# Optimization experiments

Measured on AMD Instinct MI355X. Metric: run time of the kernel, lower is better.

The kernel has to match this reference:

```python
import jax, jax.numpy as jnp
import numpy as np
import math

HEADS = 8

def setup_inputs() -> dict:
    key = jax.random.key(0)
    k1, k2 = jax.random.split(key)
    B, C, H, W = 8, 512, 32, 32
    x = jax.random.normal(k1, (B, C, H, W), dtype=jnp.float32)
    # weight-norm 1x1 conv params: v ~ N(0, 0.05), g initialized to ||v|| (torch weight_norm default)
    proj_v = jax.random.normal(k2, (3 * C, C), dtype=jnp.float32) * 0.05
    proj_g = jnp.linalg.norm(proj_v, axis=1)
    proj_b = jnp.zeros((3 * C,), dtype=jnp.float32)
    return {"x": x, "proj_v": proj_v, "proj_g": proj_g, "proj_b": proj_b}

def reference(x, proj_v, proj_g, proj_b):
    B, C, H, W = x.shape
    heads = HEADS
    dim = C // heads
    N = H * W
    # weight-normalized 1x1 conv: w = g * v / ||v|| per output channel
    w = proj_g[:, None] * proj_v / jnp.linalg.norm(proj_v, axis=1, keepdims=True)
    c = jnp.einsum('oc,bchw->bohw', w, x) + proj_b[None, :, None, None]
    c = c.reshape(B, 3, heads, dim, N)
    q, k, v = c[:, 0], c[:, 1], c[:, 2]  # each (B, heads, dim, N)
    scale = 1.0 / math.sqrt(dim)
    attn = jnp.einsum('bhdq,bhdk->bhqk', q, k) * scale  # (B, heads, N, N)
    attn = jax.nn.softmax(attn, axis=-1)
    out = jnp.einsum('bhdk,bhqk->bhdq', v, attn)  # (B, heads, dim, N)
    return x + out.reshape(B, C, H, W)
```

## Files before the change

kernel.cpp:

```cpp
#include <hip/hip_runtime.h>

typedef _Float16 f16;
typedef _Float16 f16x2 __attribute__((ext_vector_type(2)));
typedef _Float16 f16x4 __attribute__((ext_vector_type(4)));
typedef _Float16 f16x8 __attribute__((ext_vector_type(8)));
typedef float f32x4 __attribute__((ext_vector_type(4)));
typedef unsigned int u32;

__device__ inline f32x4 mfma16(f16x8 a, f16x8 b, f32x4 c) {
    return __builtin_amdgcn_mfma_f32_16x16x32_f16(a, b, c, 0, 0, 0);
}

__device__ inline f16x2 pk2(float a, float b) {
    return __builtin_bit_cast(f16x2, __builtin_amdgcn_cvt_pkrtz(a, b));
}

__device__ inline void st8(f16* p, f16x8 v) {
    *(f16x4*)p = __builtin_shufflevector(v, v, 0, 1, 2, 3);
    *(f16x4*)(p + 4) = __builtin_shufflevector(v, v, 4, 5, 6, 7);
}
__device__ inline f16x8 ld8(const f16* p) {
    f16x4 lo = *(const f16x4*)p;
    f16x4 hi = *(const f16x4*)(p + 4);
    return __builtin_shufflevector(lo, hi, 0, 1, 2, 3, 4, 5, 6, 7);
}

__device__ inline void gl2lds16(const f16* g, f16* l) {
    __builtin_amdgcn_global_load_lds(
        (const __attribute__((address_space(1))) u32*)g,
        (__attribute__((address_space(3))) u32*)l, 16, 0, 0);
}

__global__ __launch_bounds__(256) void compute_w_k(const float* __restrict__ pv,
                                                   const float* __restrict__ pg,
                                                   f16* __restrict__ w) {
    int o = blockIdx.x;
    const float* row = pv + (size_t)o * 512;
    float s = 0.f;
    for (int c = threadIdx.x; c < 512; c += 256) { float t = row[c]; s += t * t; }
    for (int off = 32; off; off >>= 1) s += __shfl_down(s, off, 64);
    __shared__ float red[4];
    int lane = threadIdx.x & 63, wid = threadIdx.x >> 6;
    if (lane == 0) red[wid] = s;
    __syncthreads();
    float tot = red[0] + red[1] + red[2] + red[3];
    float scale = pg[o] * rsqrtf(tot);
    for (int c = threadIdx.x; c < 512; c += 256)
        w[(size_t)o * 512 + c] = (f16)(row[c] * scale);
}

__global__ __launch_bounds__(256) void transpose_x_k(const float* __restrict__ x,
                                                     f16* __restrict__ xT) {
    __shared__ float t[32][33];
    int b = blockIdx.z, n0 = blockIdx.x * 32, c0 = blockIdx.y * 32;
    int tx = threadIdx.x, ty = threadIdx.y;
    const float* xb = x + (size_t)b * 512 * 1024;
    for (int i = 0; i < 4; i++)
        t[ty + 8 * i][tx] = xb[(size_t)(c0 + ty + 8 * i) * 1024 + n0 + tx];
    __syncthreads();
    f16* xTb = xT + (size_t)b * 1024 * 512;
    for (int i = 0; i < 4; i++)
        xTb[(size_t)(n0 + ty + 8 * i) * 512 + c0 + tx] = (f16)t[tx][ty + 8 * i];
}

__global__ __launch_bounds__(256) void qkv_gemm_k(const f16* __restrict__ w,
                                                  const f16* __restrict__ xT,
                                                  const float* __restrict__ pb,
                                                  f16* __restrict__ qk,
                                                  f16* __restrict__ v) {
    __shared__ f16 lA[2][128 * 64];
    __shared__ f16 lB[2][128 * 64];
    int b = blockIdx.z;
    int oBase = blockIdx.y * 128;
    int nBase = blockIdx.x * 128;
    const f16* xb = xT + (size_t)b * 1024 * 512;
    int tid = threadIdx.x, lane = tid & 63, warp = tid >> 6;
    int wy = warp >> 1, wx = warp & 1;
    int quad = lane >> 4, l15 = lane & 15;

    int srow = lane >> 3;
    int schunk = (lane & 7) ^ srow;
    const f16* aS[4]; const f16* bS[4]; int dOff[4];
    for (int j = 0; j < 4; j++) {
        int rb = (warp * 4 + j) * 8;
        aS[j] = w  + (size_t)(oBase + rb + srow) * 512 + schunk * 8;
        bS[j] = xb + (size_t)(nBase + rb + srow) * 512 + schunk * 8;
        dOff[j] = rb * 64;
    }
    int ph0 = (quad ^ (l15 & 7)) * 8;
    int ph1 = ((4 + quad) ^ (l15 & 7)) * 8;

    for (int j = 0; j < 4; j++) {
        gl2lds16(aS[j], &lA[0][dOff[j]]);
        gl2lds16(bS[j], &lB[0][dOff[j]]);
    }

    f32x4 acc[4][4] = {};

    for (int i = 0; i < 8; i++) {
        __syncthreads();
        if (i < 7) {
            int k0 = (i + 1) * 64, bb = (i + 1) & 1;
            for (int j = 0; j < 4; j++) {
                gl2lds16(aS[j] + k0, &lA[bb][dOff[j]]);
                gl2lds16(bS[j] + k0, &lB[bb][dOff[j]]);
            }
        }
        const f16* cA = lA[i & 1];
        const f16* cB = lB[i & 1];
        for (int kh = 0; kh < 2; kh++) {
            int ph = kh ? ph1 : ph0;
            f16x8 af[4], bf[4];
            for (int mi = 0; mi < 4; mi++)
                af[mi] = *(f16x8*)&cA[(wy * 64 + mi * 16 + l15) * 64 + ph];
            for (int ni = 0; ni < 4; ni++)
                bf[ni] = *(f16x8*)&cB[(wx * 64 + ni * 16 + l15) * 64 + ph];
            for (int mi = 0; mi < 4; mi++)
                for (int ni = 0; ni < 4; ni++)
                    acc[mi][ni] = mfma16(af[mi], bf[ni], acc[mi][ni]);
        }
    }

    int selB = oBase >> 9;
    for (int mi = 0; mi < 4; mi++) {
        int oRow = oBase + wy * 64 + mi * 16 + quad * 4;
        int h = (oRow >> 6) & 7, d0 = oRow & 63;
        for (int ni = 0; ni < 4; ni++) {
            int n = nBase + wx * 64 + ni * 16 + l15;
            if (selB < 2) {
                float sc = selB == 0 ? 0.125f : 1.0f;
                f16x4 o4;
                o4[0] = (f16)((acc[mi][ni][0] + pb[oRow + 0]) * sc);
                o4[1] = (f16)((acc[mi][ni][1] + pb[oRow + 1]) * sc);
                o4[2] = (f16)((acc[mi][ni][2] + pb[oRow + 2]) * sc);
                o4[3] = (f16)((acc[mi][ni][3] + pb[oRow + 3]) * sc);
                *(f16x4*)&qk[((((size_t)b * 2 + selB) * 8 + h) * 1024 + n) * 64 + d0] = o4;
            } else {
                for (int reg = 0; reg < 4; reg++) {
                    float val = acc[mi][ni][reg] + pb[oRow + reg];
                    v[(((size_t)b * 8 + h) * 64 + d0 + reg) * 1024 + n] = (f16)val;
                }
            }
        }
    }
}

#define ALDK 68
__global__ __launch_bounds__(256) void attn_k(const f16* __restrict__ qk,
                                              const f16* __restrict__ vg,
                                              const float* __restrict__ x,
                                              float* __restrict__ out) {
    __shared__ __align__(16) f16 smem[3 * 64 * ALDK];
    f16* lK = smem;
    f16* lV = smem + 64 * ALDK;
    f16* lPb = smem + 2 * 64 * ALDK;
    float* OT = (float*)smem;

    int bh = blockIdx.y;
    int b = bh >> 3, h = bh & 7;
    int qBase = blockIdx.x * 64;
    int tid = threadIdx.x, lane = tid & 63, warp = tid >> 6;
    int quad = lane >> 4, l15 = lane & 15;

    const f16* qbase = qk + (((size_t)b * 2 + 0) * 8 + h) * 1024 * 64;
    const f16* kbase = qk + (((size_t)b * 2 + 1) * 8 + h) * 1024 * 64;
    const f16* vbase = vg + ((size_t)b * 8 + h) * 64 * 1024;
    f16* lP = lPb + warp * 16 * ALDK;

    int q0 = qBase + warp * 16;
    f16x8 aq[2];
    for (int kh = 0; kh < 2; kh++)
        aq[kh] = *(const f16x8*)&qbase[(size_t)(q0 + l15) * 64 + kh * 32 + quad * 8];

    int sr0 = tid >> 3, sc0 = (tid & 7) * 8;
    int sr1 = (tid + 256) >> 3, sc1 = sc0;

    f16x8 rK[2], rV[2];
    rK[0] = *(const f16x8*)&kbase[(size_t)sr0 * 64 + sc0];
    rK[1] = *(const f16x8*)&kbase[(size_t)sr1 * 64 + sc1];
    rV[0] = *(const f16x8*)&vbase[(size_t)sr0 * 1024 + sc0];
    rV[1] = *(const f16x8*)&vbase[(size_t)sr1 * 1024 + sc1];

    f32x4 accO[4] = {};
    float l_cur = 0.f;

    for (int kt = 0; kt < 16; kt++) {
        __syncthreads();
        st8(&lK[sr0 * ALDK + sc0], rK[0]);
        st8(&lK[sr1 * ALDK + sc1], rK[1]);
        st8(&lV[sr0 * ALDK + sc0], rV[0]);
        st8(&lV[sr1 * ALDK + sc1], rV[1]);
        __syncthreads();
        if (kt < 15) {
            const f16* kb = kbase + (size_t)(kt + 1) * 64 * 64;
            rK[0] = *(const f16x8*)&kb[(size_t)sr0 * 64 + sc0];
            rK[1] = *(const f16x8*)&kb[(size_t)sr1 * 64 + sc1];
            rV[0] = *(const f16x8*)&vbase[(size_t)sr0 * 1024 + (kt + 1) * 64 + sc0];
            rV[1] = *(const f16x8*)&vbase[(size_t)sr1 * 1024 + (kt + 1) * 64 + sc1];
        }

        f32x4 st[4] = {};
        for (int mt = 0; mt < 4; mt++)
            for (int kh = 0; kh < 2; kh++) {
                f16x8 ak = ld8(&lK[(mt * 16 + l15) * ALDK + kh * 32 + quad * 8]);
                st[mt] = mfma16(ak, aq[kh], st[mt]);
            }

        float rs0 = 0.f, rs1 = 0.f, rs2 = 0.f, rs3 = 0.f;
        for (int mt = 0; mt < 4; mt++) {
            float p0 = __expf(st[mt][0]);
            float p1 = __expf(st[mt][1]);
            float p2 = __expf(st[mt][2]);
            float p3 = __expf(st[mt][3]);
            rs0 += p0; rs1 += p1; rs2 += p2; rs3 += p3;
            f16x2 lo = pk2(p0, p1);
            f16x2 hi = pk2(p2, p3);
            f16x4 pk;
            pk[0] = lo[0]; pk[1] = lo[1]; pk[2] = hi[0]; pk[3] = hi[1];
            *(f16x4*)&lP[l15 * ALDK + mt * 16 + quad * 4] = pk;
        }
        float rs = (rs0 + rs1) + (rs2 + rs3);
        rs += __shfl_xor(rs, 16, 64);
        rs += __shfl_xor(rs, 32, 64);
        l_cur += rs;

        for (int kh = 0; kh < 2; kh++) {
            f16x8 bp = ld8(&lP[l15 * ALDK + kh * 32 + quad * 8]);
            for (int dt = 0; dt < 4; dt++) {
                f16x8 av = ld8(&lV[(dt * 16 + l15) * ALDK + kh * 32 + quad * 8]);
                accO[dt] = mfma16(av, bp, accO[dt]);
            }
        }
    }

    __syncthreads();
    float rl = 1.0f / l_cur;
    for (int dt = 0; dt < 4; dt++)
        for (int r = 0; r < 4; r++)
            OT[(dt * 16 + quad * 4 + r) * ALDK + warp * 16 + l15] = accO[dt][r] * rl;
    __syncthreads();
    for (int i = 0; i < 4; i++) {
        int cid = tid + 256 * i;
        int d = cid >> 4, qi = (cid & 15) * 4;
        float4 o4 = *(float4*)&OT[d * ALDK + qi];
        size_t gi = ((size_t)b * 512 + h * 64 + d) * 1024 + qBase + qi;
        float4 xv = *(const float4*)&x[gi];
        o4.x += xv.x; o4.y += xv.y; o4.z += xv.z; o4.w += xv.w;
        *(float4*)&out[gi] = o4;
    }
}

extern "C" void kernel_launch(void* const* d_in, const int* in_sizes, int n_in,
                              void* d_out, int out_size, void* d_ws, size_t ws_size,
                              hipStream_t stream) {
    (void)in_sizes; (void)n_in; (void)out_size; (void)ws_size;
    const float* x  = (const float*)d_in[0];
    const float* pv = (const float*)d_in[1];
    const float* pg = (const float*)d_in[2];
    const float* pb = (const float*)d_in[3];
    float* out = (float*)d_out;

    char* ws = (char*)d_ws;
    f16* w   = (f16*)(ws);
    f16* xT  = (f16*)(ws + 1572864);
    f16* qk  = (f16*)(ws + 1572864 + 8388608);
    f16* v   = (f16*)(ws + 1572864 + 8388608 + 16777216);

    hipLaunchKernelGGL(compute_w_k,  dim3(1536),      dim3(256),   0, stream, pv, pg, w);
    hipLaunchKernelGGL(transpose_x_k, dim3(32, 16, 8), dim3(32, 8), 0, stream, x, xT);
    hipLaunchKernelGGL(qkv_gemm_k,   dim3(8, 12, 8),  dim3(256),   0, stream, w, xT, pb, qk, v);
    hipLaunchKernelGGL(attn_k,       dim3(16, 64),    dim3(256),   0, stream, qk, v, x, out);
}
```

Before: 142.9 us.

## Merge prep kernels, register-stage GEMM loads, and double query rows per attention warp

Merges the weight-norm and transpose kernels into one launch with a block-index split. The QKV GEMM now stages tiles through registers into a single LDS buffer instead of issuing direct global-to-LDS loads into a double buffer. The attention kernel gives each warp 32 query rows instead of 16, so each K and V fragment read from LDS feeds twice as many MFMAs, and the grid is halved. The trade-offs are higher register pressure, fewer attention blocks, and an extra barrier in the GEMM loop.

```diff
diff --git a/kernel.cpp b/kernel.cpp
--- a/kernel.cpp
+++ b/kernel.cpp
@@ -25,42 +25,39 @@
     return __builtin_shufflevector(lo, hi, 0, 1, 2, 3, 4, 5, 6, 7);
 }
 
-__device__ inline void gl2lds16(const f16* g, f16* l) {
-    __builtin_amdgcn_global_load_lds(
-        (const __attribute__((address_space(1))) u32*)g,
-        (__attribute__((address_space(3))) u32*)l, 16, 0, 0);
-}
-
-__global__ __launch_bounds__(256) void compute_w_k(const float* __restrict__ pv,
-                                                   const float* __restrict__ pg,
-                                                   f16* __restrict__ w) {
-    int o = blockIdx.x;
-    const float* row = pv + (size_t)o * 512;
-    float s = 0.f;
-    for (int c = threadIdx.x; c < 512; c += 256) { float t = row[c]; s += t * t; }
-    for (int off = 32; off; off >>= 1) s += __shfl_down(s, off, 64);
-    __shared__ float red[4];
-    int lane = threadIdx.x & 63, wid = threadIdx.x >> 6;
-    if (lane == 0) red[wid] = s;
-    __syncthreads();
-    float tot = red[0] + red[1] + red[2] + red[3];
-    float scale = pg[o] * rsqrtf(tot);
-    for (int c = threadIdx.x; c < 512; c += 256)
-        w[(size_t)o * 512 + c] = (f16)(row[c] * scale);
-}
-
-__global__ __launch_bounds__(256) void transpose_x_k(const float* __restrict__ x,
-                                                     f16* __restrict__ xT) {
-    __shared__ float t[32][33];
-    int b = blockIdx.z, n0 = blockIdx.x * 32, c0 = blockIdx.y * 32;
-    int tx = threadIdx.x, ty = threadIdx.y;
-    const float* xb = x + (size_t)b * 512 * 1024;
-    for (int i = 0; i < 4; i++)
-        t[ty + 8 * i][tx] = xb[(size_t)(c0 + ty + 8 * i) * 1024 + n0 + tx];
-    __syncthreads();
-    f16* xTb = xT + (size_t)b * 1024 * 512;
-    for (int i = 0; i < 4; i++)
-        xTb[(size_t)(n0 + ty + 8 * i) * 512 + c0 + tx] = (f16)t[tx][ty + 8 * i];
+__global__ __launch_bounds__(256) void prep_k(const float* __restrict__ pv,
+                                              const float* __restrict__ pg,
+                                              f16* __restrict__ w,
+                                              const float* __restrict__ x,
+                                              f16* __restrict__ xT) {
+    int bid = blockIdx.x;
+    if (bid < 1536) {
+        int o = bid;
+        const float* row = pv + (size_t)o * 512;
+        float s = 0.f;
+        for (int c = threadIdx.x; c < 512; c += 256) { float t = row[c]; s += t * t; }
+        for (int off = 32; off; off >>= 1) s += __shfl_down(s, off, 64);
+        __shared__ float red[4];
+        int lane = threadIdx.x & 63, wid = threadIdx.x >> 6;
+        if (lane == 0) red[wid] = s;
+        __syncthreads();
+        float tot = red[0] + red[1] + red[2] + red[3];
+        float scale = pg[o] * rsqrtf(tot);
+        for (int c = threadIdx.x; c < 512; c += 256)
+            w[(size_t)o * 512 + c] = (f16)(row[c] * scale);
+    } else {
+        int t2 = bid - 1536;
+        int n0 = (t2 & 31) * 32, c0 = ((t2 >> 5) & 15) * 32, b = t2 >> 9;
+        int tx = threadIdx.x & 31, ty = threadIdx.x >> 5;
+        __shared__ float t[32][33];
+        const float* xb = x + (size_t)b * 512 * 1024;
+        for (int i = 0; i < 4; i++)
+            t[ty + 8 * i][tx] = xb[(size_t)(c0 + ty + 8 * i) * 1024 + n0 + tx];
+        __syncthreads();
+        f16* xTb = xT + (size_t)b * 1024 * 512;
+        for (int i = 0; i < 4; i++)
+            xTb[(size_t)(n0 + ty + 8 * i) * 512 + c0 + tx] = (f16)t[tx][ty + 8 * i];
+    }
 }
 
 __global__ __launch_bounds__(256) void qkv_gemm_k(const f16* __restrict__ w,
@@ -68,8 +65,8 @@
                                                   const float* __restrict__ pb,
                                                   f16* __restrict__ qk,
                                                   f16* __restrict__ v) {
-    __shared__ f16 lA[2][128 * 64];
-    __shared__ f16 lB[2][128 * 64];
+    __shared__ f16 lA[128 * 64];
+    __shared__ f16 lB[128 * 64];
     int b = blockIdx.z;
     int oBase = blockIdx.y * 128;
     int nBase = blockIdx.x * 128;
@@ -79,42 +76,47 @@
     int quad = lane >> 4, l15 = lane & 15;
 
     int srow = lane >> 3;
-    int schunk = (lane & 7) ^ srow;
-    const f16* aS[4]; const f16* bS[4]; int dOff[4];
+    int phys = lane & 7;
+    int schunk = phys ^ srow;
+    const f16* aS[4]; const f16* bS[4]; int ldsOff[4];
     for (int j = 0; j < 4; j++) {
         int rb = (warp * 4 + j) * 8;
         aS[j] = w  + (size_t)(oBase + rb + srow) * 512 + schunk * 8;
         bS[j] = xb + (size_t)(nBase + rb + srow) * 512 + schunk * 8;
-        dOff[j] = rb * 64;
+        ldsOff[j] = (rb + srow) * 64 + phys * 8;
     }
     int ph0 = (quad ^ (l15 & 7)) * 8;
     int ph1 = ((4 + quad) ^ (l15 & 7)) * 8;
 
+    f16x8 rA[4], rB[4];
     for (int j = 0; j < 4; j++) {
-        gl2lds16(aS[j], &lA[0][dOff[j]]);
-        gl2lds16(bS[j], &lB[0][dOff[j]]);
+        rA[j] = *(const f16x8*)aS[j];
+        rB[j] = *(const f16x8*)bS[j];
     }
 
     f32x4 acc[4][4] = {};
 
     for (int i = 0; i < 8; i++) {
         __syncthreads();
+        for (int j = 0; j < 4; j++) {
+            *(f16x8*)&lA[ldsOff[j]] = rA[j];
+            *(f16x8*)&lB[ldsOff[j]] = rB[j];
+        }
+        __syncthreads();
         if (i < 7) {
-            int k0 = (i + 1) * 64, bb = (i + 1) & 1;
+            int k0 = (i + 1) * 64;
             for (int j = 0; j < 4; j++) {
-                gl2lds16(aS[j] + k0, &lA[bb][dOff[j]]);
-                gl2lds16(bS[j] + k0, &lB[bb][dOff[j]]);
-            }
-        }
-        const f16* cA = lA[i & 1];
-        const f16* cB = lB[i & 1];
+                rA[j] = *(const f16x8*)(aS[j] + k0);
+                rB[j] = *(const f16x8*)(bS[j] + k0);
+            }
+        }
         for (int kh = 0; kh < 2; kh++) {
             int ph = kh ? ph1 : ph0;
             f16x8 af[4], bf[4];
             for (int mi = 0; mi < 4; mi++)
-                af[mi] = *(f16x8*)&cA[(wy * 64 + mi * 16 + l15) * 64 + ph];
+                af[mi] = *(f16x8*)&lA[(wy * 64 + mi * 16 + l15) * 64 + ph];
             for (int ni = 0; ni < 4; ni++)
-                bf[ni] = *(f16x8*)&cB[(wx * 64 + ni * 16 + l15) * 64 + ph];
+                bf[ni] = *(f16x8*)&lB[(wx * 64 + ni * 16 + l15) * 64 + ph];
             for (int mi = 0; mi < 4; mi++)
                 for (int ni = 0; ni < 4; ni++)
                     acc[mi][ni] = mfma16(af[mi], bf[ni], acc[mi][ni]);
@@ -150,7 +152,7 @@
                                               const f16* __restrict__ vg,
                                               const float* __restrict__ x,
                                               float* __restrict__ out) {
-    __shared__ __align__(16) f16 smem[3 * 64 * ALDK];
+    __shared__ __align__(16) f16 smem[(2 * 64 + 8 * 16) * ALDK];
     f16* lK = smem;
     f16* lV = smem + 64 * ALDK;
     f16* lPb = smem + 2 * 64 * ALDK;
@@ -158,19 +160,19 @@
 
     int bh = blockIdx.y;
     int b = bh >> 3, h = bh & 7;
-    int qBase = blockIdx.x * 64;
+    int qBase = blockIdx.x * 128;
     int tid = threadIdx.x, lane = tid & 63, warp = tid >> 6;
     int quad = lane >> 4, l15 = lane & 15;
 
     const f16* qbase = qk + (((size_t)b * 2 + 0) * 8 + h) * 1024 * 64;
     const f16* kbase = qk + (((size_t)b * 2 + 1) * 8 + h) * 1024 * 64;
     const f16* vbase = vg + ((size_t)b * 8 + h) * 64 * 1024;
-    f16* lP = lPb + warp * 16 * ALDK;
-
-    int q0 = qBase + warp * 16;
-    f16x8 aq[2];
-    for (int kh = 0; kh < 2; kh++)
-        aq[kh] = *(const f16x8*)&qbase[(size_t)(q0 + l15) * 64 + kh * 32 + quad * 8];
+
+    int q0 = qBase + warp * 32;
+    f16x8 aq[2][2];
+    for (int s = 0; s < 2; s++)
+        for (int kh = 0; kh < 2; kh++)
+            aq[s][kh] = *(const f16x8*)&qbase[(size_t)(q0 + s * 16 + l15) * 64 + kh * 32 + quad * 8];
 
     int sr0 = tid >> 3, sc0 = (tid & 7) * 8;
     int sr1 = (tid + 256) >> 3, sc1 = sc0;
@@ -181,8 +183,8 @@
     rV[0] = *(const f16x8*)&vbase[(size_t)sr0 * 1024 + sc0];
     rV[1] = *(const f16x8*)&vbase[(size_t)sr1 * 1024 + sc1];
 
-    f32x4 accO[4] = {};
-    float l_cur = 0.f;
+    f32x4 accO[2][4] = {};
+    float l_cur[2] = {0.f, 0.f};
 
     for (int kt = 0; kt < 16; kt++) {
         __syncthreads();
@@ -199,50 +201,66 @@
             rV[1] = *(const f16x8*)&vbase[(size_t)sr1 * 1024 + (kt + 1) * 64 + sc1];
         }
 
-        f32x4 st[4] = {};
-        for (int mt = 0; mt < 4; mt++)
-            for (int kh = 0; kh < 2; kh++) {
-                f16x8 ak = ld8(&lK[(mt * 16 + l15) * ALDK + kh * 32 + quad * 8]);
-                st[mt] = mfma16(ak, aq[kh], st[mt]);
-            }
-
-        float rs0 = 0.f, rs1 = 0.f, rs2 = 0.f, rs3 = 0.f;
+        f32x4 st[2][4] = {};
         for (int mt = 0; mt < 4; mt++) {
-            float p0 = __expf(st[mt][0]);
-            float p1 = __expf(st[mt][1]);
-            float p2 = __expf(st[mt][2]);
-            float p3 = __expf(st[mt][3]);
-            rs0 += p0; rs1 += p1; rs2 += p2; rs3 += p3;
-            f16x2 lo = pk2(p0, p1);
-            f16x2 hi = pk2(p2, p3);
-            f16x4 pk;
-            pk[0] = lo[0]; pk[1] = lo[1]; pk[2] = hi[0]; pk[3] = hi[1];
-            *(f16x4*)&lP[l15 * ALDK + mt * 16 + quad * 4] = pk;
-        }
-        float rs = (rs0 + rs1) + (rs2 + rs3);
-        rs += __shfl_xor(rs, 16, 64);
-        rs += __shfl_xor(rs, 32, 64);
-        l_cur += rs;
-
-        for (int kh = 0; kh < 2; kh++) {
-            f16x8 bp = ld8(&lP[l15 * ALDK + kh * 32 + quad * 8]);
-            for (int dt = 0; dt < 4; dt++) {
-                f16x8 av = ld8(&lV[(dt * 16 + l15) * ALDK + kh * 32 + quad * 8]);
-                accO[dt] = mfma16(av, bp, accO[dt]);
+            f16x8 ak0 = ld8(&lK[(mt * 16 + l15) * ALDK + 0 * 32 + quad * 8]);
+            f16x8 ak1 = ld8(&lK[(mt * 16 + l15) * ALDK + 1 * 32 + quad * 8]);
+            for (int s = 0; s < 2; s++) {
+                st[s][mt] = mfma16(ak0, aq[s][0], st[s][mt]);
+                st[s][mt] = mfma16(ak1, aq[s][1], st[s][mt]);
+            }
+        }
+
+        for (int s = 0; s < 2; s++) {
+            f16* lP = lPb + (warp * 2 + s) * 16 * ALDK;
+            float rs0 = 0.f, rs1 = 0.f, rs2 = 0.f, rs3 = 0.f;
+            for (int mt = 0; mt < 4; mt++) {
+                float p0 = __expf(st[s][mt][0]);
+                float p1 = __expf(st[s][mt][1]);
+                float p2 = __expf(st[s][mt][2]);
+                float p3 = __expf(st[s][mt][3]);
+                rs0 += p0; rs1 += p1; rs2 += p2; rs3 += p3;
+                f16x2 lo = pk2(p0, p1);
+                f16x2 hi = pk2(p2, p3);
+                f16x4 pk;
+                pk[0] = lo[0]; pk[1] = lo[1]; pk[2] = hi[0]; pk[3] = hi[1];
+                *(f16x4*)&lP[l15 * ALDK + mt * 16 + quad * 4] = pk;
+            }
+            float rs = (rs0 + rs1) + (rs2 + rs3);
+            rs += __shfl_xor(rs, 16, 64);
+            rs += __shfl_xor(rs, 32, 64);
+            l_cur[s] += rs;
+        }
+
+        f16x8 bp[2][2];
+        for (int s = 0; s < 2; s++) {
+            f16* lP = lPb + (warp * 2 + s) * 16 * ALDK;
+            bp[s][0] = ld8(&lP[l15 * ALDK + 0 * 32 + quad * 8]);
+            bp[s][1] = ld8(&lP[l15 * ALDK + 1 * 32 + quad * 8]);
+        }
+        for (int dt = 0; dt < 4; dt++) {
+            f16x8 av0 = ld8(&lV[(dt * 16 + l15) * ALDK + 0 * 32 + quad * 8]);
+            f16x8 av1 = ld8(&lV[(dt * 16 + l15) * ALDK + 1 * 32 + quad * 8]);
+            for (int s = 0; s < 2; s++) {
+                accO[s][dt] = mfma16(av0, bp[s][0], accO[s][dt]);
+                accO[s][dt] = mfma16(av1, bp[s][1], accO[s][dt]);
             }
         }
     }
 
     __syncthreads();
-    float rl = 1.0f / l_cur;
-    for (int dt = 0; dt < 4; dt++)
-        for (int r = 0; r < 4; r++)
-            OT[(dt * 16 + quad * 4 + r) * ALDK + warp * 16 + l15] = accO[dt][r] * rl;
+    for (int s = 0; s < 2; s++) {
+        float rl = 1.0f / l_cur[s];
+        for (int dt = 0; dt < 4; dt++)
+            for (int r = 0; r < 4; r++)
+                OT[(dt * 16 + quad * 4 + r) * 132 + warp * 32 + s * 16 + l15] =
+                    accO[s][dt][r] * rl;
+    }
     __syncthreads();
-    for (int i = 0; i < 4; i++) {
+    for (int i = 0; i < 8; i++) {
         int cid = tid + 256 * i;
-        int d = cid >> 4, qi = (cid & 15) * 4;
-        float4 o4 = *(float4*)&OT[d * ALDK + qi];
+        int d = cid >> 5, qi = (cid & 31) * 4;
+        float4 o4 = *(float4*)&OT[d * 132 + qi];
         size_t gi = ((size_t)b * 512 + h * 64 + d) * 1024 + qBase + qi;
         float4 xv = *(const float4*)&x[gi];
         o4.x += xv.x; o4.y += xv.y; o4.z += xv.z; o4.w += xv.w;
@@ -266,8 +284,7 @@
     f16* qk  = (f16*)(ws + 1572864 + 8388608);
     f16* v   = (f16*)(ws + 1572864 + 8388608 + 16777216);
 
-    hipLaunchKernelGGL(compute_w_k,  dim3(1536),      dim3(256),   0, stream, pv, pg, w);
-    hipLaunchKernelGGL(transpose_x_k, dim3(32, 16, 8), dim3(32, 8), 0, stream, x, xT);
-    hipLaunchKernelGGL(qkv_gemm_k,   dim3(8, 12, 8),  dim3(256),   0, stream, w, xT, pb, qk, v);
-    hipLaunchKernelGGL(attn_k,       dim3(16, 64),    dim3(256),   0, stream, qk, v, x, out);
-}
+    hipLaunchKernelGGL(prep_k,     dim3(5632),     dim3(256), 0, stream, pv, pg, w, x, xT);
+    hipLaunchKernelGGL(qkv_gemm_k, dim3(8, 12, 8), dim3(256), 0, stream, w, xT, pb, qk, v);
+    hipLaunchKernelGGL(attn_k,     dim3(8, 64),    dim3(256), 0, stream, qk, v, x, out);
+}
```

New measurement: 137.3 us. 1.04x faster.
